# Performance work log

Hardware: AMD Instinct MI355X
Metric: run time of the kernel (lower is better)

Reference implementation:

```python
import jax, jax.numpy as jnp
import numpy as np

H_SHEET, W_SHEET = 150, 300
N = H_SHEET * W_SHEET          # 45000 neurons
K = 32                         # synapses per neuron
STD = 10.0                     # connectivity std
T = 100                        # num_timesteps
B = 32                         # batch size


def setup_inputs() -> dict:
    rng = np.random.default_rng(0)
    ii = np.repeat(np.arange(H_SHEET), W_SHEET)   # (N,) row coord
    jj = np.tile(np.arange(W_SHEET), H_SHEET)     # (N,) col coord
    # Gaussian topographic synapses, clamped to the sheet (duplicates allowed;
    # summing duplicates via segment_sum == coalesced spmm).
    si = np.clip((rng.standard_normal((N, K)) * STD + ii[:, None]).astype(np.int64), 0, H_SHEET - 1)
    sj = np.clip((rng.standard_normal((N, K)) * STD + jj[:, None]).astype(np.int64), 0, W_SHEET - 1)
    syn = si * W_SHEET + sj                        # (N,K) synapse (row) indices
    root = ii * W_SHEET + jj                       # (N,) neuron's own flat index
    rows = np.concatenate([syn, root[:, None]], axis=1).reshape(-1)  # entry row = synapse
    cols = np.repeat(root, K + 1)                                    # entry col = root neuron

    key = jax.random.key(0)
    k1, k2, k3, k4 = jax.random.split(key, 4)
    nnz = rows.size
    vals = jax.random.normal(k1, (nnz,), dtype=jnp.float32) * np.float32(np.sqrt(2.0 / K))
    x = jax.random.normal(k2, (B, N), dtype=jnp.float32)
    bias = jnp.zeros((N,), jnp.float32)
    w1 = jax.random.normal(k3, (N, 64), dtype=jnp.float32) * np.float32(1.0 / np.sqrt(N))
    b1 = jnp.zeros((64,), jnp.float32)
    w2 = jax.random.normal(k4, (64, 10), dtype=jnp.float32) * np.float32(1.0 / 8.0)
    b2 = jnp.zeros((10,), jnp.float32)
    return {
        "x": x, "vals": vals, "bias": bias,
        "w1": w1, "b1": b1, "w2": w2, "b2": b2,
        "rows": jnp.asarray(rows, jnp.int32),
        "cols": jnp.asarray(cols, jnp.int32),
    }


def reference(x, vals, bias, w1, b1, w2, b2, rows, cols):
    # x: (B, N). Cell operates batch-last: h is (N, B).
    h = x.T

    def step(h, _):
        # spmm: out[r] = sum_{entries e with rows[e]==r} vals[e] * h[cols[e]]
        msg = vals[:, None] * h[cols]                       # (nnz, B)
        y = jax.ops.segment_sum(msg, rows, num_segments=N)  # (N, B)
        return jax.nn.relu(y + bias[:, None]), None

    h, _ = jax.lax.scan(step, h, None, length=T)
    h = h.T                                                 # (B, N)
    # out_block: Linear(N,64) -> relu -> Linear(64,10)
    return jax.nn.relu(h @ w1 + b1) @ w2 + b2
```

## Files before the change

kernel.cpp:

```cpp
#include <hip/hip_runtime.h>
#include <hip/hip_bf16.h>
#include <hip/hip_fp16.h>

#define H_SHEET 150
#define W_SHEET 300
#define NN      (H_SHEET * W_SHEET)
#define KSYN    32
#define KP1     33
#define NNZ     (NN * KP1)
#define BATCH   32
#define TSTEPS  100
#define NPAD    45056
#define NCHUNK  64
#define NPART   ((NN + NCHUNK - 1) / NCHUNK)
#define LONG_THRESH 64

typedef float vf4 __attribute__((ext_vector_type(4)));

#define ROWS_PER_BLOCK 32
#define SGRID ((NN + ROWS_PER_BLOCK - 1) / ROWS_PER_BLOCK)
#define LGRID 1024

__device__ inline int xcd_swizzle(int bid, int nwg) {
    int q = nwg >> 3, r = nwg & 7;
    int xcd = bid & 7, idx = bid >> 3;
    return (xcd < r ? xcd * (q + 1) : r * (q + 1) + (xcd - r) * q) + idx;
}

__device__ inline float unpack_val(unsigned int e) {
    return __half2float(__ushort_as_half((unsigned short)(e >> 16)));
}
__device__ inline int unpack_col(unsigned int e, int r) {
    return r + (int)(short)(unsigned short)(e & 0xffffu);
}

__global__ __launch_bounds__(256) void hist_kernel(const int* __restrict__ rows,
                                                   int* __restrict__ counts) {
    int e = blockIdx.x * 256 + threadIdx.x;
    if (e < NNZ) atomicAdd(&counts[rows[e]], 1);
}

__global__ __launch_bounds__(1024) void scan_kernel(const int* __restrict__ counts,
                                                    int* __restrict__ row_ptr) {
    __shared__ int wsum[16];
    __shared__ int carry_s;
    const int lane = threadIdx.x & 63;
    const int wid  = threadIdx.x >> 6;
    if (threadIdx.x == 0) carry_s = 0;
    __syncthreads();
    for (int base = 0; base < NN; base += 1024) {
        int i = base + threadIdx.x;
        int v = (i < NN) ? counts[i] : 0;
        int incl = v;
        #pragma unroll
        for (int d = 1; d < 64; d <<= 1) {
            int t = __shfl_up(incl, d, 64);
            if (lane >= d) incl += t;
        }
        if (lane == 63) wsum[wid] = incl;
        __syncthreads();
        if (wid == 0 && lane < 16) {
            int s = wsum[lane];
            #pragma unroll
            for (int d = 1; d < 16; d <<= 1) {
                int t = __shfl_up(s, d, 64);
                if (lane >= d) s += t;
            }
            wsum[lane] = s;
        }
        __syncthreads();
        int wprev = (wid > 0) ? wsum[wid - 1] : 0;
        int total = carry_s + wprev + incl;
        if (i < NN) row_ptr[i + 1] = total;
        __syncthreads();
        if (threadIdx.x == 1023) carry_s += wsum[15];
        __syncthreads();
    }
    if (threadIdx.x == 0) row_ptr[0] = 0;
}

__global__ __launch_bounds__(256) void scatter_kernel(const int* __restrict__ rows,
                                                      const float* __restrict__ vals,
                                                      int* __restrict__ cursor,
                                                      unsigned int* __restrict__ csr4) {
    int e = blockIdx.x * 256 + threadIdx.x;
    if (e >= NNZ) return;
    int r = rows[e];
    int pos = atomicAdd(&cursor[r], 1);
    int col = e / KP1;
    int d = col - r;
    unsigned short hv = __half_as_ushort(__float2half(vals[e]));
    csr4[pos] = (unsigned int)(unsigned short)(short)d | ((unsigned int)hv << 16);
}

__global__ __launch_bounds__(256) void classify_kernel(const int* __restrict__ row_ptr,
                                                       int* __restrict__ long_list,
                                                       int* __restrict__ long_cnt) {
    int r = blockIdx.x * 256 + threadIdx.x;
    if (r >= NN) return;
    int n = row_ptr[r + 1] - row_ptr[r];
    if (n > LONG_THRESH) long_list[atomicAdd(long_cnt, 1)] = r;
}

__global__ __launch_bounds__(256) void init_kernel(const float* __restrict__ x,
                                                   float* __restrict__ h) {
    __shared__ float tile[64 * 33];
    int n0 = blockIdx.x * 64;
    int tn = threadIdx.x & 63;
    int tb = threadIdx.x >> 6;
    #pragma unroll
    for (int p = 0; p < 8; ++p) {
        int b = tb + p * 4;
        int n = n0 + tn;
        float v = (n < NN) ? x[b * NN + n] : 0.f;
        tile[tn * 33 + b] = v;
    }
    __syncthreads();
    int b2 = threadIdx.x & 31;
    int nb = threadIdx.x >> 5;
    #pragma unroll
    for (int p = 0; p < 8; ++p) {
        int n = n0 + nb + p * 8;
        if (n < NN) h[n * 32 + b2] = tile[(nb + p * 8) * 33 + b2];
    }
}

__global__ __launch_bounds__(256) void step_kernel(const int* __restrict__ row_ptr,
                                                   const unsigned int* __restrict__ csr4,
                                                   const float* __restrict__ bias,
                                                   const float* __restrict__ h_in,
                                                   float* __restrict__ h_out,
                                                   const int* __restrict__ long_list,
                                                   const int* __restrict__ long_cnt) {
    if (blockIdx.x < SGRID) {
        int blk = xcd_swizzle(blockIdx.x, SGRID);
        int r = blk * ROWS_PER_BLOCK + (threadIdx.x >> 3);
        if (r >= NN) return;
        int bo = (threadIdx.x & 7) * 4;

        int s = row_ptr[r];
        int e = row_ptr[r + 1];
        int n = e - s;
        if (n > LONG_THRESH) return;
        const unsigned int* __restrict__ p = csr4 + s;

        vf4 accA = (vf4)(0.f);
        vf4 accB = (vf4)(0.f);
        int i = 0;
        for (; i + 8 <= n; i += 8) {
            unsigned int e0 = p[i];
            unsigned int e1 = p[i + 1];
            unsigned int e2 = p[i + 2];
            unsigned int e3 = p[i + 3];
            unsigned int e4 = p[i + 4];
            unsigned int e5 = p[i + 5];
            unsigned int e6 = p[i + 6];
            unsigned int e7 = p[i + 7];
            vf4 h0 = *(const vf4*)&h_in[(unpack_col(e0, r) << 5) + bo];
            vf4 h1 = *(const vf4*)&h_in[(unpack_col(e1, r) << 5) + bo];
            vf4 h2 = *(const vf4*)&h_in[(unpack_col(e2, r) << 5) + bo];
            vf4 h3 = *(const vf4*)&h_in[(unpack_col(e3, r) << 5) + bo];
            vf4 h4 = *(const vf4*)&h_in[(unpack_col(e4, r) << 5) + bo];
            vf4 h5 = *(const vf4*)&h_in[(unpack_col(e5, r) << 5) + bo];
            vf4 h6 = *(const vf4*)&h_in[(unpack_col(e6, r) << 5) + bo];
            vf4 h7 = *(const vf4*)&h_in[(unpack_col(e7, r) << 5) + bo];
            accA += unpack_val(e0) * h0;
            accB += unpack_val(e1) * h1;
            accA += unpack_val(e2) * h2;
            accB += unpack_val(e3) * h3;
            accA += unpack_val(e4) * h4;
            accB += unpack_val(e5) * h5;
            accA += unpack_val(e6) * h6;
            accB += unpack_val(e7) * h7;
        }
        for (; i < n; ++i) {
            unsigned int e0 = p[i];
            vf4 hv = *(const vf4*)&h_in[(unpack_col(e0, r) << 5) + bo];
            accA += unpack_val(e0) * hv;
        }
        vf4 acc = accA + accB;
        float bv = bias[r];
        vf4 o;
        o.x = fmaxf(acc.x + bv, 0.f);
        o.y = fmaxf(acc.y + bv, 0.f);
        o.z = fmaxf(acc.z + bv, 0.f);
        o.w = fmaxf(acc.w + bv, 0.f);
        *(vf4*)&h_out[(r << 5) + bo] = o;
    } else {
        __shared__ vf4 red[256];
        const int lcnt = *long_cnt;
        const int g  = threadIdx.x >> 3;
        const int bq = threadIdx.x & 7;
        const int bo = bq * 4;
        for (int li = (int)blockIdx.x - SGRID; li < lcnt; li += LGRID) {
            int r = long_list[li];
            int s = row_ptr[r];
            int n = row_ptr[r + 1] - s;
            const unsigned int* __restrict__ p = csr4 + s;
            vf4 acc = (vf4)(0.f);
            for (int i = g; i < n; i += 32) {
                unsigned int e0 = p[i];
                vf4 hv = *(const vf4*)&h_in[(unpack_col(e0, r) << 5) + bo];
                acc += unpack_val(e0) * hv;
            }
            red[threadIdx.x] = acc;
            __syncthreads();
            if (threadIdx.x < 64) {
                vf4 a = red[threadIdx.x] + red[threadIdx.x + 64] +
                        red[threadIdx.x + 128] + red[threadIdx.x + 192];
                red[threadIdx.x] = a;
            }
            __syncthreads();
            if (threadIdx.x < 8) {
                vf4 a = (vf4)(0.f);
                #pragma unroll
                for (int k = 0; k < 8; ++k) a += red[k * 8 + threadIdx.x];
                float bv = bias[r];
                vf4 o;
                o.x = fmaxf(a.x + bv, 0.f);
                o.y = fmaxf(a.y + bv, 0.f);
                o.z = fmaxf(a.z + bv, 0.f);
                o.w = fmaxf(a.w + bv, 0.f);
                *(vf4*)&h_out[(r << 5) + threadIdx.x * 4] = o;
            }
            __syncthreads();
        }
    }
}

__global__ __launch_bounds__(256) void gemm1_kernel(const float* __restrict__ h,
                                                    const float* __restrict__ w1,
                                                    float* __restrict__ partials) {
    int n0 = blockIdx.x * NCHUNK;
    int nend = n0 + NCHUNK; if (nend > NN) nend = NN;
    int j  = threadIdx.x & 63;
    int b0 = threadIdx.x >> 6;
    float sum[8];
    #pragma unroll
    for (int ii = 0; ii < 8; ++ii) sum[ii] = 0.f;
    for (int n = n0; n < nend; ++n) {
        float w = w1[n * 64 + j];
        #pragma unroll
        for (int ii = 0; ii < 8; ++ii)
            sum[ii] = fmaf(w, h[n * 32 + b0 + ii * 4], sum[ii]);
    }
    float* dst = partials + blockIdx.x * 2048;
    #pragma unroll
    for (int ii = 0; ii < 8; ++ii)
        dst[(b0 + ii * 4) * 64 + j] = sum[ii];
}

__global__ __launch_bounds__(256) void gemm1_reduce(const float* __restrict__ partials,
                                                    float* __restrict__ acc) {
    int cell = blockIdx.x * 256 + threadIdx.x;
    float s0 = 0.f, s1 = 0.f, s2 = 0.f, s3 = 0.f;
    int k = 0;
    for (; k + 4 <= NPART; k += 4) {
        s0 += partials[(k + 0) * 2048 + cell];
        s1 += partials[(k + 1) * 2048 + cell];
        s2 += partials[(k + 2) * 2048 + cell];
        s3 += partials[(k + 3) * 2048 + cell];
    }
    for (; k < NPART; ++k) s0 += partials[k * 2048 + cell];
    acc[cell] = (s0 + s1) + (s2 + s3);
}

__global__ __launch_bounds__(320) void head_kernel(const float* __restrict__ acc,
                                                   const float* __restrict__ b1,
                                                   const float* __restrict__ w2,
                                                   const float* __restrict__ b2,
                                                   float* __restrict__ out) {
    int t = threadIdx.x;
    if (t >= 320) return;
    int b = t / 10, oj = t % 10;
    float s = b2[oj];
    #pragma unroll
    for (int k = 0; k < 64; ++k)
        s += fmaxf(acc[b * 64 + k] + b1[k], 0.f) * w2[k * 10 + oj];
    out[b * 10 + oj] = s;
}

extern "C" void kernel_launch(void* const* d_in, const int* in_sizes, int n_in,
                              void* d_out, int out_size, void* d_ws, size_t ws_size,
                              hipStream_t stream) {
    const float* x    = (const float*)d_in[0];
    const float* vals = (const float*)d_in[1];
    const float* bias = (const float*)d_in[2];
    const float* w1   = (const float*)d_in[3];
    const float* b1   = (const float*)d_in[4];
    const float* w2   = (const float*)d_in[5];
    const float* b2   = (const float*)d_in[6];
    const int*   rows = (const int*)d_in[7];
    float* out = (float*)d_out;

    const int NB = NN * BATCH;
    float*        hA        = (float*)d_ws;
    float*        hB        = hA + NB;
    int*          row_ptr   = (int*)(hB + NB);
    int*          cursor    = row_ptr + NPAD;
    unsigned int* csr4      = (unsigned int*)(cursor + NPAD);
    float*        partials  = (float*)(csr4 + NNZ);
    float*        acc       = partials + NPART * 2048;
    int*          long_cnt  = (int*)(acc + 2048);
    int*          long_list = long_cnt + 8;

    hipMemsetAsync(cursor, 0, NN * sizeof(int), stream);
    hipMemsetAsync(long_cnt, 0, sizeof(int), stream);
    hist_kernel<<<(NNZ + 255) / 256, 256, 0, stream>>>(rows, cursor);
    scan_kernel<<<1, 1024, 0, stream>>>(cursor, row_ptr);
    hipMemcpyAsync(cursor, row_ptr, NN * sizeof(int), hipMemcpyDeviceToDevice, stream);
    scatter_kernel<<<(NNZ + 255) / 256, 256, 0, stream>>>(rows, vals, cursor, csr4);
    classify_kernel<<<(NN + 255) / 256, 256, 0, stream>>>(row_ptr, long_list, long_cnt);

    init_kernel<<<(NN + 63) / 64, 256, 0, stream>>>(x, hA);

    float* bufs[2] = { hA, hB };
    for (int t = 0; t < TSTEPS; ++t) {
        step_kernel<<<SGRID + LGRID, 256, 0, stream>>>(
            row_ptr, csr4, bias, bufs[t & 1], bufs[(t + 1) & 1],
            long_list, long_cnt);
    }
    float* hfin = bufs[TSTEPS & 1];

    gemm1_kernel<<<NPART, 256, 0, stream>>>(hfin, w1, partials);
    gemm1_reduce<<<8, 256, 0, stream>>>(partials, acc);
    head_kernel<<<1, 320, 0, stream>>>(acc, b1, w2, b2, out);
}
```

Before: 2.654 ms.

## Fuse all timesteps into one persistent kernel with grid-wide atomic barriers

Replaces the 100 per-timestep step_kernel launches with a single persistent kernel of 704 blocks of 512 threads. Each block owns 64 rows, keeps its row pointers and bias in registers across steps, and synchronises with the other blocks through per-step atomic counters in global memory. This removes per-launch overhead and the launch gaps between steps, and reloads row metadata only once. In exchange, every block must be co-resident (704 blocks at up to 6 per CU), and each step now ends with a spin barrier whose cost grows with the number of blocks.

Result: slower. 8.852 ms (+233.5%).

```diff
diff --git a/kernel.cpp b/kernel.cpp
--- a/kernel.cpp
+++ b/kernel.cpp
@@ -17,9 +17,9 @@
 
 typedef float vf4 __attribute__((ext_vector_type(4)));
 
-#define ROWS_PER_BLOCK 32
-#define SGRID ((NN + ROWS_PER_BLOCK - 1) / ROWS_PER_BLOCK)
-#define LGRID 1024
+#define PBLOCKS      704
+#define PTHREADS     512
+#define ROWS_PER_PB  64
 
 __device__ inline int xcd_swizzle(int bid, int nwg) {
     int q = nwg >> 3, r = nwg & 7;
@@ -125,103 +125,122 @@
     }
 }
 
-__global__ __launch_bounds__(256) void step_kernel(const int* __restrict__ row_ptr,
-                                                   const unsigned int* __restrict__ csr4,
-                                                   const float* __restrict__ bias,
-                                                   const float* __restrict__ h_in,
-                                                   float* __restrict__ h_out,
-                                                   const int* __restrict__ long_list,
-                                                   const int* __restrict__ long_cnt) {
-    if (blockIdx.x < SGRID) {
-        int blk = xcd_swizzle(blockIdx.x, SGRID);
-        int r = blk * ROWS_PER_BLOCK + (threadIdx.x >> 3);
-        if (r >= NN) return;
-        int bo = (threadIdx.x & 7) * 4;
-
-        int s = row_ptr[r];
-        int e = row_ptr[r + 1];
-        int n = e - s;
-        if (n > LONG_THRESH) return;
-        const unsigned int* __restrict__ p = csr4 + s;
-
-        vf4 accA = (vf4)(0.f);
-        vf4 accB = (vf4)(0.f);
-        int i = 0;
-        for (; i + 8 <= n; i += 8) {
-            unsigned int e0 = p[i];
-            unsigned int e1 = p[i + 1];
-            unsigned int e2 = p[i + 2];
-            unsigned int e3 = p[i + 3];
-            unsigned int e4 = p[i + 4];
-            unsigned int e5 = p[i + 5];
-            unsigned int e6 = p[i + 6];
-            unsigned int e7 = p[i + 7];
-            vf4 h0 = *(const vf4*)&h_in[(unpack_col(e0, r) << 5) + bo];
-            vf4 h1 = *(const vf4*)&h_in[(unpack_col(e1, r) << 5) + bo];
-            vf4 h2 = *(const vf4*)&h_in[(unpack_col(e2, r) << 5) + bo];
-            vf4 h3 = *(const vf4*)&h_in[(unpack_col(e3, r) << 5) + bo];
-            vf4 h4 = *(const vf4*)&h_in[(unpack_col(e4, r) << 5) + bo];
-            vf4 h5 = *(const vf4*)&h_in[(unpack_col(e5, r) << 5) + bo];
-            vf4 h6 = *(const vf4*)&h_in[(unpack_col(e6, r) << 5) + bo];
-            vf4 h7 = *(const vf4*)&h_in[(unpack_col(e7, r) << 5) + bo];
-            accA += unpack_val(e0) * h0;
-            accB += unpack_val(e1) * h1;
-            accA += unpack_val(e2) * h2;
-            accB += unpack_val(e3) * h3;
-            accA += unpack_val(e4) * h4;
-            accB += unpack_val(e5) * h5;
-            accA += unpack_val(e6) * h6;
-            accB += unpack_val(e7) * h7;
-        }
-        for (; i < n; ++i) {
-            unsigned int e0 = p[i];
-            vf4 hv = *(const vf4*)&h_in[(unpack_col(e0, r) << 5) + bo];
-            accA += unpack_val(e0) * hv;
-        }
-        vf4 acc = accA + accB;
-        float bv = bias[r];
-        vf4 o;
-        o.x = fmaxf(acc.x + bv, 0.f);
-        o.y = fmaxf(acc.y + bv, 0.f);
-        o.z = fmaxf(acc.z + bv, 0.f);
-        o.w = fmaxf(acc.w + bv, 0.f);
-        *(vf4*)&h_out[(r << 5) + bo] = o;
-    } else {
-        __shared__ vf4 red[256];
-        const int lcnt = *long_cnt;
-        const int g  = threadIdx.x >> 3;
-        const int bq = threadIdx.x & 7;
-        const int bo = bq * 4;
-        for (int li = (int)blockIdx.x - SGRID; li < lcnt; li += LGRID) {
-            int r = long_list[li];
-            int s = row_ptr[r];
-            int n = row_ptr[r + 1] - s;
-            const unsigned int* __restrict__ p = csr4 + s;
-            vf4 acc = (vf4)(0.f);
-            for (int i = g; i < n; i += 32) {
+__global__ __launch_bounds__(PTHREADS, 6) void rnn_persistent(
+        const int* __restrict__ row_ptr, const unsigned int* __restrict__ csr4,
+        const float* __restrict__ bias, float* __restrict__ hA,
+        float* __restrict__ hB, const int* __restrict__ long_list,
+        const int* __restrict__ long_cnt, int* __restrict__ bar) {
+    __shared__ vf4 red[PTHREADS];
+
+    const int blk   = xcd_swizzle(blockIdx.x, PBLOCKS);
+    const int slot  = threadIdx.x >> 3;
+    const int lane8 = threadIdx.x & 7;
+    const int bo    = lane8 * 4;
+    const int r     = blk * ROWS_PER_PB + slot;
+
+    bool active = (r < NN);
+    int s = 0, n = 0;
+    float bv = 0.f;
+    if (active) {
+        s  = row_ptr[r];
+        n  = row_ptr[r + 1] - s;
+        bv = bias[r];
+        if (n > LONG_THRESH) active = false;
+    }
+    const unsigned int* __restrict__ p = csr4 + s;
+    const int lcnt = *long_cnt;
+
+    for (int t = 0; t < TSTEPS; ++t) {
+        const float* __restrict__ hin  = (t & 1) ? hB : hA;
+        float*       __restrict__ hout = (t & 1) ? hA : hB;
+
+        if (active) {
+            vf4 accA = (vf4)(0.f);
+            vf4 accB = (vf4)(0.f);
+            int i = 0;
+            for (; i + 8 <= n; i += 8) {
                 unsigned int e0 = p[i];
-                vf4 hv = *(const vf4*)&h_in[(unpack_col(e0, r) << 5) + bo];
-                acc += unpack_val(e0) * hv;
-            }
-            red[threadIdx.x] = acc;
-            __syncthreads();
-            if (threadIdx.x < 64) {
-                vf4 a = red[threadIdx.x] + red[threadIdx.x + 64] +
-                        red[threadIdx.x + 128] + red[threadIdx.x + 192];
-                red[threadIdx.x] = a;
+                unsigned int e1 = p[i + 1];
+                unsigned int e2 = p[i + 2];
+                unsigned int e3 = p[i + 3];
+                unsigned int e4 = p[i + 4];
+                unsigned int e5 = p[i + 5];
+                unsigned int e6 = p[i + 6];
+                unsigned int e7 = p[i + 7];
+                vf4 h0 = *(const vf4*)&hin[(unpack_col(e0, r) << 5) + bo];
+                vf4 h1 = *(const vf4*)&hin[(unpack_col(e1, r) << 5) + bo];
+                vf4 h2 = *(const vf4*)&hin[(unpack_col(e2, r) << 5) + bo];
+                vf4 h3 = *(const vf4*)&hin[(unpack_col(e3, r) << 5) + bo];
+                vf4 h4 = *(const vf4*)&hin[(unpack_col(e4, r) << 5) + bo];
+                vf4 h5 = *(const vf4*)&hin[(unpack_col(e5, r) << 5) + bo];
+                vf4 h6 = *(const vf4*)&hin[(unpack_col(e6, r) << 5) + bo];
+                vf4 h7 = *(const vf4*)&hin[(unpack_col(e7, r) << 5) + bo];
+                accA += unpack_val(e0) * h0;
+                accB += unpack_val(e1) * h1;
+                accA += unpack_val(e2) * h2;
+                accB += unpack_val(e3) * h3;
+                accA += unpack_val(e4) * h4;
+                accB += unpack_val(e5) * h5;
+                accA += unpack_val(e6) * h6;
+                accB += unpack_val(e7) * h7;
+            }
+            for (; i < n; ++i) {
+                unsigned int e0 = p[i];
+                vf4 hv = *(const vf4*)&hin[(unpack_col(e0, r) << 5) + bo];
+                accA += unpack_val(e0) * hv;
+            }
+            vf4 acc = accA + accB;
+            vf4 o;
+            o.x = fmaxf(acc.x + bv, 0.f);
+            o.y = fmaxf(acc.y + bv, 0.f);
+            o.z = fmaxf(acc.z + bv, 0.f);
+            o.w = fmaxf(acc.w + bv, 0.f);
+            *(vf4*)&hout[(r << 5) + bo] = o;
+        }
+
+        for (int li = (int)blockIdx.x; li < lcnt; li += PBLOCKS) {
+            int lr = long_list[li];
+            int ls = row_ptr[lr];
+            int ln = row_ptr[lr + 1] - ls;
+            const unsigned int* __restrict__ lp = csr4 + ls;
+            int g = threadIdx.x >> 3;
+            vf4 a = (vf4)(0.f);
+            for (int i = g; i < ln; i += 64) {
+                unsigned int e0 = lp[i];
+                vf4 hv = *(const vf4*)&hin[(unpack_col(e0, lr) << 5) + bo];
+                a += unpack_val(e0) * hv;
+            }
+            red[threadIdx.x] = a;
+            __syncthreads();
+            if (threadIdx.x < 128) {
+                red[threadIdx.x] = red[threadIdx.x] + red[threadIdx.x + 128] +
+                                   red[threadIdx.x + 256] + red[threadIdx.x + 384];
             }
             __syncthreads();
             if (threadIdx.x < 8) {
-                vf4 a = (vf4)(0.f);
+                vf4 aa = (vf4)(0.f);
                 #pragma unroll
-                for (int k = 0; k < 8; ++k) a += red[k * 8 + threadIdx.x];
-                float bv = bias[r];
+                for (int k = 0; k < 16; ++k) aa += red[k * 8 + threadIdx.x];
+                float lbv = bias[lr];
                 vf4 o;
-                o.x = fmaxf(a.x + bv, 0.f);
-                o.y = fmaxf(a.y + bv, 0.f);
-                o.z = fmaxf(a.z + bv, 0.f);
-                o.w = fmaxf(a.w + bv, 0.f);
-                *(vf4*)&h_out[(r << 5) + threadIdx.x * 4] = o;
+                o.x = fmaxf(aa.x + lbv, 0.f);
+                o.y = fmaxf(aa.y + lbv, 0.f);
+                o.z = fmaxf(aa.z + lbv, 0.f);
+                o.w = fmaxf(aa.w + lbv, 0.f);
+                *(vf4*)&hout[(lr << 5) + threadIdx.x * 4] = o;
+            }
+            __syncthreads();
+        }
+
+        if (t + 1 < TSTEPS) {
+            __syncthreads();
+            if (threadIdx.x == 0) {
+                __hip_atomic_fetch_add(&bar[t], 1, __ATOMIC_RELEASE,
+                                       __HIP_MEMORY_SCOPE_AGENT);
+                while (__hip_atomic_fetch_add(&bar[t], 0, __ATOMIC_RELAXED,
+                                              __HIP_MEMORY_SCOPE_AGENT) < PBLOCKS)
+                    __builtin_amdgcn_s_sleep(8);
+                __builtin_amdgcn_fence(__ATOMIC_ACQUIRE, "agent");
             }
             __syncthreads();
         }
@@ -303,9 +322,11 @@
     float*        acc       = partials + NPART * 2048;
     int*          long_cnt  = (int*)(acc + 2048);
     int*          long_list = long_cnt + 8;
+    int*          bar       = long_list + NPAD;
 
     hipMemsetAsync(cursor, 0, NN * sizeof(int), stream);
     hipMemsetAsync(long_cnt, 0, sizeof(int), stream);
+    hipMemsetAsync(bar, 0, TSTEPS * sizeof(int), stream);
     hist_kernel<<<(NNZ + 255) / 256, 256, 0, stream>>>(rows, cursor);
     scan_kernel<<<1, 1024, 0, stream>>>(cursor, row_ptr);
     hipMemcpyAsync(cursor, row_ptr, NN * sizeof(int), hipMemcpyDeviceToDevice, stream);
@@ -314,13 +335,9 @@
 
     init_kernel<<<(NN + 63) / 64, 256, 0, stream>>>(x, hA);
 
-    float* bufs[2] = { hA, hB };
-    for (int t = 0; t < TSTEPS; ++t) {
-        step_kernel<<<SGRID + LGRID, 256, 0, stream>>>(
-            row_ptr, csr4, bias, bufs[t & 1], bufs[(t + 1) & 1],
-            long_list, long_cnt);
-    }
-    float* hfin = bufs[TSTEPS & 1];
+    rnn_persistent<<<PBLOCKS, PTHREADS, 0, stream>>>(
+        row_ptr, csr4, bias, hA, hB, long_list, long_cnt, bar);
+    float* hfin = hA;
 
     gemm1_kernel<<<NPART, 256, 0, stream>>>(hfin, w1, partials);
     gemm1_reduce<<<8, 256, 0, stream>>>(partials, acc);
```
